# Performance work log

Measured on AMD Instinct MI355X. Metric: run time of the kernel, lower is better.

The kernel has to match this reference:

```python
import jax, jax.numpy as jnp
import numpy as np


def _conv_relu(x, w, b):
    # Conv2d ksize=5, stride=1, padding=2 (same), dilation=1, then ReLU
    y = jax.lax.conv_general_dilated(x, w, window_strides=(1, 1), padding=[(2, 2), (2, 2)],
                                     dimension_numbers=("NCHW", "OIHW", "NCHW"))
    return jax.nn.relu(y + b[None, :, None, None])


def setup_inputs():
    B, S, C, M, BERT = 4, 128, 49, 288, 768
    ks = jax.random.split(jax.random.key(0), 12)
    return {
        "bert_output": jax.random.normal(ks[0], (B, S, BERT), jnp.float32),
        "memory_embs": jax.random.normal(ks[1], (B, S, C, M), jnp.float32),
        "mem_length": jax.random.randint(ks[2], (B, S, 1), 0, C + 1).astype(jnp.int32),
        "cn_concept_weights": jax.random.normal(ks[3], (B, S, C), jnp.float32),
        "ignore_no_memory_token": 1,
        "concept_size": C,
        "W_lin1": jax.random.normal(ks[4], (M, BERT), jnp.float32) * 0.02,
        "b_lin1": jnp.zeros((M,), jnp.float32),
        "sentinel": jax.random.normal(ks[5], (M,), jnp.float32) * 0.02,
        "weight1": jax.random.normal(ks[6], (M, C + 1), jnp.float32) * 0.05,
        "weight2": jax.random.normal(ks[7], (M, C + 1), jnp.float32) * 0.05,
        "conv1_w": jax.random.normal(ks[8], (S, S, 5, 5), jnp.float32) * 0.02,
        "conv1_b": jnp.zeros((S,), jnp.float32),
        "conv2_w": jax.random.normal(ks[9], (S, S, 5, 5), jnp.float32) * 0.02,
        "conv2_b": jnp.zeros((S,), jnp.float32),
        "ln_g": jnp.ones((144,), jnp.float32),
        "ln_b": jnp.zeros((144,), jnp.float32),
        "W_out": jax.random.normal(ks[10], (300, 144), jnp.float32) * 0.05,
        "b_out": jnp.zeros((300,), jnp.float32),
    }


def reference(bert_output, memory_embs, mem_length, cn_concept_weights,
              ignore_no_memory_token, concept_size,
              W_lin1, b_lin1, sentinel, weight1, weight2,
              conv1_w, conv1_b, conv2_w, conv2_b, ln_g, ln_b, W_out, b_out):
    B, S, _ = bert_output.shape
    C = concept_size
    M = sentinel.shape[0]
    eb = bert_output @ W_lin1.T + b_lin1                                   # [B,S,M]
    # add_sentinel: prepend sentinel row, extended_memory [B,S,C+1,M]
    ext_mem = jnp.concatenate([jnp.broadcast_to(sentinel, (B, S, 1, M)), memory_embs], axis=2)
    # expanded_bert[b,s,t,:] = eb[b,t,:]; avoid materializing it via einsum
    attn_w = jnp.einsum("btm,bsjm->bstj", eb, ext_mem)                     # [B,S,S,C+1]
    score = attn_w.mean(axis=2)                                            # [B,S,C+1]
    ordinal = jnp.arange(C + 1, dtype=jnp.float32)
    score = score + (mem_length.astype(jnp.float32) < ordinal).astype(jnp.float32) * (-1e6)
    cw = jnp.concatenate([jnp.zeros((B, S, 1), jnp.float32), cn_concept_weights], axis=2)
    score = 0.7 * jax.nn.softmax(score, axis=2) + 0.3 * jax.nn.softmax(cw, axis=2)
    # top-k threshold mask (keep >= 5th largest), then softmax over masked scores
    thr = jax.lax.top_k(score, 5)[0][..., 4:5]
    score = score * (score >= thr).astype(score.dtype)
    att = jax.nn.softmax(score, axis=2)                                    # [B,S,C+1]
    # torch: matmul of att repeated along last dim with ext_mem
    # == att[...,i] * sum_j ext_mem[...,j,:]
    summ = att[..., None] * ext_mem.sum(axis=2)[:, :, None, :]             # [B,S,C+1,M]
    # einsum 'b s a m, n c -> b s n m' is an outer product of the a-sum with the c-sum
    t1 = summ.sum(axis=2)                                                  # [B,S,M]
    t2 = jnp.einsum("bst,btm->bsm", attn_w.sum(axis=3), eb)                # sum_a (AW^T @ EB)
    cwt = (weight1.sum(axis=1)[None, None, :, None] * t1[:, :, None, :]
           + weight2.sum(axis=1)[None, None, :, None] * t2[:, :, None, :])  # [B,S,M,M]
    cwt = jax.nn.softmax(jnp.tanh(cwt), axis=2)
    summ = jnp.einsum("bsam,bsmn->bsan", summ, cwt)                        # [B,S,C+1,M]
    # self_coding: conv(S->S) -> maxpool2 -> conv -> LayerNorm(144) -> mean over dim2 -> Linear(144,300)
    x = _conv_relu(summ, conv1_w, conv1_b)
    x = jax.lax.reduce_window(x, -jnp.inf, jax.lax.max, (1, 1, 2, 2), (1, 1, 2, 2), "VALID")
    x = _conv_relu(x, conv2_w, conv2_b)                                    # [B,S,(C+1)//2,144]
    mu = x.mean(axis=-1, keepdims=True)
    var = ((x - mu) ** 2).mean(axis=-1, keepdims=True)
    x = (x - mu) / jnp.sqrt(var + 1e-5) * ln_g + ln_b
    x = x.mean(axis=2)                                                     # [B,S,144]
    out = x @ W_out.T + b_out                                              # [B,S,300]
    if ignore_no_memory_token:
        out = out * (mem_length > 0).astype(out.dtype)                     # [B,S,1] broadcast
    return out
```

## Files before the change

kernel.cpp:

```cpp
#include <hip/hip_runtime.h>

#define B_    4
#define S_    128
#define BERT_ 768
#define C_    49
#define C1_   50
#define M_    288
#define HP_   25
#define WP_   144
#define NOUT_ 300

typedef short bf16x8 __attribute__((ext_vector_type(8)));
typedef short short4v __attribute__((ext_vector_type(4)));
typedef float f32x4 __attribute__((ext_vector_type(4)));

static __device__ __forceinline__ short f2bf(float f) {
  unsigned u = __float_as_uint(f);
  unsigned r = (u + 0x7fffu + ((u >> 16) & 1u)) >> 16;
  return (short)r;
}
static __device__ __forceinline__ float bf2f(short v) {
  return __uint_as_float(((unsigned)(unsigned short)v) << 16);
}
static __device__ __forceinline__ unsigned cvt_pk_bf16(float lo, float hi) {
  unsigned r;
  asm("v_cvt_pk_bf16_f32 %0, %1, %2" : "=v"(r) : "v"(lo), "v"(hi));
  return r;
}

static __device__ __forceinline__ void cast_body(const float* src, short* dst,
                                                 long loOff, int R, int Ks, int Kd, int idx)
{
  if (idx >= R * Kd) return;
  int k = idx % Kd, r = idx / Kd;
  short h = 0, l = 0;
  if (k < Ks) {
    float v = src[(long)r * Ks + k];
    h = f2bf(v);
    l = f2bf(v - bf2f(h));
  }
  dst[idx] = h;
  dst[idx + loOff] = l;
}
static __device__ __forceinline__ void wperm_body(const float* w, short* wq, int r)
{
  if (r >= 128 * 128) return;
  int o = r >> 7, ch = r & 127;
  int chq = ch >> 3, e = ch & 7;
  const float* src = &w[(long)r * 25];
#pragma unroll
  for (int tap = 0; tap < 25; ++tap)
    wq[(((long)(tap * 16 + chq)) * 128 + o) * 8 + e] = f2bf(src[tap]);
}
__global__ __launch_bounds__(256) void prep_kernel(
    const float* __restrict__ bert, short* __restrict__ bertb,
    const float* __restrict__ W1, short* __restrict__ w1b,
    const float* __restrict__ Wo, short* __restrict__ wob,
    const float* __restrict__ c1w, short* __restrict__ w1p,
    const float* __restrict__ c2w, short* __restrict__ w2p,
    const float* __restrict__ w1m, const float* __restrict__ w2m,
    float* __restrict__ w1s, float* __restrict__ w2s)
{
  const int g = blockIdx.x, tid = threadIdx.x;
  if (g < 1536)       cast_body(bert, bertb, 393216L, 512, 768, 768, g * 256 + tid);
  else if (g < 2400)  cast_body(W1, w1b, 221184L, 288, 768, 768, (g - 1536) * 256 + tid);
  else if (g < 2700)  cast_body(Wo, wob, 76800L, 300, 144, 256, (g - 2400) * 256 + tid);
  else if (g < 2764)  wperm_body(c1w, w1p, (g - 2700) * 256 + tid);
  else if (g < 2828)  wperm_body(c2w, w2p, (g - 2764) * 256 + tid);
  else {
    int m = (g - 2828) * 256 + tid;
    if (m < M_) {
      float a = 0.f, b = 0.f;
      for (int c = 0; c < C1_; ++c) { a += w1m[m * C1_ + c]; b += w2m[m * C1_ + c]; }
      w1s[m] = a; w2s[m] = b;
    }
  }
}

template<int OMODE>
__global__ __launch_bounds__(256) void gemm_split(
    const short* __restrict__ A, const short* __restrict__ Bm,
    const float* __restrict__ bias,
    float* __restrict__ Outf, short* __restrict__ Outb,
    int Mr, int Nc, int KH,
    long aB, int aP, long aLo,
    long bB, int bP, long bLo,
    long oB, int oP,
    long obB, int obP, long obLo,
    const int* __restrict__ ml, const int* __restrict__ ign)
{
  const int z = blockIdx.z;
  const int i0 = blockIdx.y * 64, j0 = blockIdx.x * 64;
  __shared__ __attribute__((aligned(16))) short As[2][64 * 64];
  __shared__ __attribute__((aligned(16))) short Bs[2][64 * 64];
  const int tid = threadIdx.x;
  const int wave = tid >> 6, lane = tid & 63;
  const int lr = lane & 15, kq = lane >> 4;
  f32x4 acc[4] = {};
  const short* Ab = A + z * aB;
  const short* Bb = Bm + z * bB;
  const bf16x8 vz = {0, 0, 0, 0, 0, 0, 0, 0};
  for (int kh = 0; kh < KH; ++kh) {
    if (kh) __syncthreads();
    for (int u = tid; u < 512; u += 256) {
      int row = u >> 3, c = u & 7;
      int gi = i0 + row;
      const short* src = &Ab[(long)gi * aP + kh * 64 + c * 8];
      bf16x8 vh = (gi < Mr) ? *(const bf16x8*)src : vz;
      bf16x8 vl = (gi < Mr) ? *(const bf16x8*)(src + aLo) : vz;
      int dst = row * 64 + ((c ^ (row & 7)) * 8);
      *(bf16x8*)&As[0][dst] = vh;
      *(bf16x8*)&As[1][dst] = vl;
    }
    for (int u = tid; u < 512; u += 256) {
      int row = u >> 3, c = u & 7;
      int gj = j0 + row;
      const short* src = &Bb[(long)gj * bP + kh * 64 + c * 8];
      bf16x8 vh = (gj < Nc) ? *(const bf16x8*)src : vz;
      bf16x8 vl = (gj < Nc) ? *(const bf16x8*)(src + bLo) : vz;
      int dst = row * 64 + ((c ^ (row & 7)) * 8);
      *(bf16x8*)&Bs[0][dst] = vh;
      *(bf16x8*)&Bs[1][dst] = vl;
    }
    __syncthreads();
#pragma unroll
    for (int ks = 0; ks < 2; ++ks) {
      const int ch = ks * 4 + kq;
      const int ar = wave * 16 + lr;
      const int ao = ar * 64 + ((ch ^ (ar & 7)) * 8);
      bf16x8 ah = *(const bf16x8*)&As[0][ao];
      bf16x8 al = *(const bf16x8*)&As[1][ao];
#pragma unroll
      for (int ni = 0; ni < 4; ++ni) {
        const int br = ni * 16 + lr;
        const int bo2 = br * 64 + ((ch ^ (br & 7)) * 8);
        bf16x8 bh = *(const bf16x8*)&Bs[0][bo2];
        bf16x8 bl = *(const bf16x8*)&Bs[1][bo2];
        acc[ni] = __builtin_amdgcn_mfma_f32_16x16x32_bf16(ah, bh, acc[ni], 0, 0, 0);
        acc[ni] = __builtin_amdgcn_mfma_f32_16x16x32_bf16(ah, bl, acc[ni], 0, 0, 0);
        acc[ni] = __builtin_amdgcn_mfma_f32_16x16x32_bf16(al, bh, acc[ni], 0, 0, 0);
      }
    }
  }
#pragma unroll
  for (int ni = 0; ni < 4; ++ni) {
    int jg = j0 + ni * 16 + lr;
    if (jg >= Nc) continue;
#pragma unroll
    for (int r = 0; r < 4; ++r) {
      int ig = i0 + wave * 16 + kq * 4 + r;
      if (ig >= Mr) continue;
      float v = acc[ni][r];
      if (bias) v += bias[jg];
      if constexpr (OMODE == 0 || OMODE == 1)
        Outf[z * oB + (long)ig * oP + jg] = v;
      if constexpr (OMODE == 1) {
        long o = ((long)((ig >> 7) * 288 + jg)) * 128 + (ig & 127);
        short h = f2bf(v);
        Outb[o] = h;
        Outb[o + obLo] = f2bf(v - bf2f(h));
      }
      if constexpr (OMODE == 2) {
        long o = z * obB + (long)ig * obP + jg;
        short h = f2bf(v);
        Outb[o] = h;
        Outb[o + obLo] = f2bf(v - bf2f(h));
      }
      if constexpr (OMODE == 3) {
        if (ign[0] != 0 && ml[ig] <= 0) v = 0.f;
        Outf[z * oB + (long)ig * oP + jg] = v;
      }
    }
  }
}

__global__ __launch_bounds__(256) void ebbar_kernel(
    const float* __restrict__ eb, float* __restrict__ ebb)
{
  const int chunk = blockIdx.x, b = blockIdx.y;
  const int tid = threadIdx.x;
  const int ml_ = tid & 63, sg = tid >> 6;
  const int m = chunk * 64 + ml_;
  __shared__ float sP[4][64];
  float s = 0.f;
  if (m < M_) {
    const float* p = eb + ((long)(b * S_ + sg * 32)) * M_ + m;
    for (int t = 0; t < 32; ++t) s += p[(long)t * M_];
  }
  sP[sg][ml_] = s;
  __syncthreads();
  if (sg == 0 && m < M_)
    ebb[b * M_ + m] = (sP[0][ml_] + sP[1][ml_] + sP[2][ml_] + sP[3][ml_]) * (1.f / (float)S_);
}

__global__ __launch_bounds__(256) void score_kernel(
    const float* __restrict__ mem, const float* __restrict__ sentinel,
    const float* __restrict__ ebbar, const float* __restrict__ cw,
    const int* __restrict__ ml, float* __restrict__ E, short* __restrict__ Eb,
    float* __restrict__ attTp)
{
  const int s = blockIdx.x, b = blockIdx.y;
  const int tid = threadIdx.x, wave = tid >> 6, lane = tid & 63;
  __shared__ float sEb[M_];
  __shared__ float sE[4][M_];
  __shared__ float sScore[C1_];
  for (int m = tid; m < M_; m += 256) sEb[m] = ebbar[b * M_ + m];
  __syncthreads();

  const float* base = mem + ((long)(b * S_ + s)) * C_ * M_;
  float Ereg[5] = {0.f, 0.f, 0.f, 0.f, 0.f};
  for (int jj = wave; jj < C_; jj += 4) {
    const float* row = base + (long)jj * M_;
    float d = 0.f;
#pragma unroll
    for (int q = 0; q < 5; ++q) {
      int m = lane + q * 64;
      if (m < M_) { float v = row[m]; Ereg[q] += v; d = fmaf(v, sEb[m], d); }
    }
#pragma unroll
    for (int off = 32; off; off >>= 1) d += __shfl_down(d, off, 64);
    if (lane == 0) sScore[jj + 1] = d;
  }
#pragma unroll
  for (int q = 0; q < 5; ++q) { int m = lane + q * 64; if (m < M_) sE[wave][m] = Ereg[q]; }
  __syncthreads();

  if (wave == 0) {
    float d0 = 0.f;
    for (int m = lane; m < M_; m += 64) d0 = fmaf(sentinel[m], sEb[m], d0);
#pragma unroll
    for (int off = 32; off; off >>= 1) d0 += __shfl_down(d0, off, 64);
    if (lane == 0) sScore[0] = d0;
  }
  for (int m = tid; m < M_; m += 256) {
    float ev = sentinel[m] + sE[0][m] + sE[1][m] + sE[2][m] + sE[3][m];
    E[((long)(b * S_ + s)) * M_ + m] = ev;
    short h = f2bf(ev);
    Eb[((long)(b * S_ + s)) * 384 + m] = h;
    Eb[196608 + ((long)(b * S_ + s)) * 384 + m] = f2bf(ev - bf2f(h));
  }
  __syncthreads();

  if (wave == 0) {
    const int mlv = ml[b * S_ + s];
    float sc = (lane < C1_) ? sScore[lane] : 0.f;
    if (lane < C1_ && mlv < lane) sc -= 1e6f;
    float mx = (lane < C1_) ? sc : -3.0e38f;
#pragma unroll
    for (int off = 32; off; off >>= 1) mx = fmaxf(mx, __shfl_xor(mx, off, 64));
    float e1 = (lane < C1_) ? __expf(sc - mx) : 0.f;
    float s1 = e1;
#pragma unroll
    for (int off = 32; off; off >>= 1) s1 += __shfl_xor(s1, off, 64);
    float p1 = e1 / s1;
    float cv = 0.f;
    if (lane >= 1 && lane < C1_) cv = cw[((long)(b * S_ + s)) * C_ + lane - 1];
    float mx2 = (lane < C1_) ? cv : -3.0e38f;
#pragma unroll
    for (int off = 32; off; off >>= 1) mx2 = fmaxf(mx2, __shfl_xor(mx2, off, 64));
    float e2 = (lane < C1_) ? __expf(cv - mx2) : 0.f;
    float s2 = e2;
#pragma unroll
    for (int off = 32; off; off >>= 1) s2 += __shfl_xor(s2, off, 64);
    float p2 = e2 / s2;
    float scm = 0.7f * p1 + 0.3f * p2;
    bool active = (lane < C1_);
    float thr = 0.f;
    for (int r = 0; r < 5; ++r) {
      float v = active ? scm : -3.0e38f;
      int idx = lane;
#pragma unroll
      for (int off = 32; off; off >>= 1) {
        float ov = __shfl_xor(v, off, 64);
        int oi = __shfl_xor(idx, off, 64);
        if (ov > v || (ov == v && oi < idx)) { v = ov; idx = oi; }
      }
      thr = v;
      if (lane == idx) active = false;
    }
    float kept = (lane < C1_ && scm >= thr) ? scm : 0.f;
    float mx3 = (lane < C1_) ? kept : -3.0e38f;
#pragma unroll
    for (int off = 32; off; off >>= 1) mx3 = fmaxf(mx3, __shfl_xor(mx3, off, 64));
    float e3 = (lane < C1_) ? __expf(kept - mx3) : 0.f;
    float s3 = e3;
#pragma unroll
    for (int off = 32; off; off >>= 1) s3 += __shfl_xor(s3, off, 64);
    if (lane < C1_) attTp[((long)(b * 54) + lane + 2) * 128 + s] = e3 / s3;
  }
}

__global__ __launch_bounds__(576) void g_kernel(
    const float* __restrict__ E, const float* __restrict__ t2,
    const float* __restrict__ w1s, const float* __restrict__ w2s,
    short* __restrict__ Gt)
{
  const int s = blockIdx.x, b = blockIdx.y;
  __shared__ float sE[M_], s1[M_], s2[M_];
  const int tid = threadIdx.x;
  const long base = (long)(b * S_ + s) * M_;
  for (int m = tid; m < M_; m += 576) { sE[m] = E[base + m]; s1[m] = w1s[m]; s2[m] = w2s[m]; }
  __syncthreads();
  const int n = tid >> 1, half = tid & 1;
  const float a = sE[n];
  const float c = t2[base + n];
  float num = 0.f, den = 0.f;
  const int m0 = half * 144;
#pragma unroll 4
  for (int mm = 0; mm < 144; ++mm) {
    int m = m0 + mm;
    float z = fmaf(s1[m], a, s2[m] * c);
    float u = __expf(2.f * z);
    float th = 1.f - 2.f / (u + 1.f);
    float e = __expf(th);
    num = fmaf(sE[m], e, num);
    den += e;
  }
  num += __shfl_xor(num, 1, 64);
  den += __shfl_xor(den, 1, 64);
  if (half == 0)
    Gt[((long)(b * 292) + 2 + n) * 128 + s] = f2bf(num / den);
}

__global__ __launch_bounds__(256) void conv1_aw(
    const short* __restrict__ w1q, const float* __restrict__ attp,
    short* __restrict__ AWq)
{
  const int b = blockIdx.z, h = blockIdx.y, half = blockIdx.x;
  __shared__ float sAtt[5][128];
  const int tid = threadIdx.x;
  for (int u = tid; u < 640; u += 256)
    sAtt[u >> 7][u & 127] = attp[((long)(b * 54) + h + (u >> 7)) * 128 + (u & 127)];
  __syncthreads();
  const long obase = ((long)(b * 50 + h) * 80) * 1024;
  for (int u = tid; u < 5120; u += 256) {
    int c = half * 40 + (u >> 7);
    int o = u & 127;
    int dw = c / 16, chq = c & 15;
    float acc[8] = {};
#pragma unroll
    for (int dh = 0; dh < 5; ++dh) {
      bf16x8 wv = *(const bf16x8*)&w1q[(((long)((dh * 5 + dw) * 16 + chq)) * 128 + o) * 8];
      const float* ar = &sAtt[dh][chq * 8];
#pragma unroll
      for (int e = 0; e < 8; ++e) acc[e] = fmaf(bf2f(wv[e]), ar[e], acc[e]);
    }
    union { unsigned u4[4]; bf16x8 v; } pk;
    pk.u4[0] = cvt_pk_bf16(acc[0], acc[1]);
    pk.u4[1] = cvt_pk_bf16(acc[2], acc[3]);
    pk.u4[2] = cvt_pk_bf16(acc[4], acc[5]);
    pk.u4[3] = cvt_pk_bf16(acc[6], acc[7]);
    *(bf16x8*)&AWq[obase + (long)c * 1024 + o * 8] = pk.v;
  }
}

__global__ __launch_bounds__(256) void conv1_mfma(
    const short* __restrict__ AWq, const short* __restrict__ Gt,
    const float* __restrict__ bias, short* __restrict__ y1t)
{
  const int b = blockIdx.z, hrow = blockIdx.y;
  const int w0 = blockIdx.x * 144;
  __shared__ __attribute__((aligned(16))) short Bs[2][148 * 64];
  const int tid = threadIdx.x;
  const int wave = tid >> 6, lane = tid & 63;
  const int lr = lane & 15, kq = lane >> 4;
  f32x4 acc[2][9] = {};

  const short* src = Gt + ((long)(b * 292) + w0) * 128;
  for (int u = tid; u < 2368; u += 256) {
    int row = u >> 4, c = u & 15;
    bf16x8 v = *(const bf16x8*)&src[row * 128 + c * 8];
    *(bf16x8*)&Bs[c >> 3][row * 64 + (((c & 7) ^ (row & 7)) * 8)] = v;
  }
  __syncthreads();

  const long awb = (long)(b * 50 + hrow) * 80;
  for (int dw = 0; dw < 5; ++dw) {
#pragma unroll
    for (int ks = 0; ks < 4; ++ks) {
      const int ch = ks * 4 + kq;
      const long abase = (awb + dw * 16 + ch) * 128 + wave * 32 + lr;
      bf16x8 af0 = *(const bf16x8*)&AWq[abase * 8];
      bf16x8 af1 = *(const bf16x8*)&AWq[(abase + 16) * 8];
      const int arr = ch >> 3, cc = ch & 7;
#pragma unroll
      for (int ni = 0; ni < 9; ++ni) {
        const int row = lr + ni * 16 + dw;
        bf16x8 bfr = *(const bf16x8*)&Bs[arr][row * 64 + ((cc ^ (row & 7)) * 8)];
        acc[0][ni] = __builtin_amdgcn_mfma_f32_16x16x32_bf16(af0, bfr, acc[0][ni], 0, 0, 0);
        acc[1][ni] = __builtin_amdgcn_mfma_f32_16x16x32_bf16(af1, bfr, acc[1][ni], 0, 0, 0);
      }
    }
  }
#pragma unroll
  for (int mi = 0; mi < 2; ++mi) {
    const int og = wave * 32 + mi * 16 + kq * 4;
#pragma unroll
    for (int ni = 0; ni < 9; ++ni) {
      int wg = w0 + ni * 16 + lr;
      short4v pk;
#pragma unroll
      for (int r = 0; r < 4; ++r)
        pk[r] = f2bf(fmaxf(acc[mi][ni][r] + bias[og + r], 0.f));
      *(short4v*)&y1t[(((long)(b * 50) + hrow) * 288 + wg) * 128 + og] = pk;
    }
  }
}

__global__ __launch_bounds__(256) void conv2_dh(
    const short* __restrict__ wq,
    const short* __restrict__ act,
    short* __restrict__ y2p)
{
  constexpr int NREP = 3;
  const int bz = blockIdx.z;
  const int b = bz / 5, dh = bz % 5;
  const int hp = blockIdx.y;
  const int w0 = blockIdx.x * 48;
  __shared__ __attribute__((aligned(16))) short Bs[2][52 * 64];
  const int tid = threadIdx.x;
  const int wave = tid >> 6, lane = tid & 63;
  const int lr = lane & 15, kq = lane >> 4;
  f32x4 acc[2][NREP] = {};

  const short* src = act + (((long)(b * 29) + hp + dh) * 148 + w0) * 128;
  for (int u = tid; u < 832; u += 256) {
    int row = u >> 4, c = u & 15;
    bf16x8 v = *(const bf16x8*)&src[row * 128 + c * 8];
    *(bf16x8*)&Bs[c >> 3][row * 64 + (((c & 7) ^ (row & 7)) * 8)] = v;
  }
  __syncthreads();

#pragma unroll
  for (int dw = 0; dw < 5; ++dw) {
    const int tap = dh * 5 + dw;
#pragma unroll
    for (int ks = 0; ks < 4; ++ks) {
      const int ch = ks * 4 + kq;
      const long abase = ((long)(tap * 16 + ch)) * 128 + wave * 32 + lr;
      bf16x8 af0 = *(const bf16x8*)&wq[abase * 8];
      bf16x8 af1 = *(const bf16x8*)&wq[(abase + 16) * 8];
      const int arr = ch >> 3, cc = ch & 7;
#pragma unroll
      for (int ni = 0; ni < NREP; ++ni) {
        const int row = lr + ni * 16 + dw;
        bf16x8 bfr = *(const bf16x8*)&Bs[arr][row * 64 + ((cc ^ (row & 7)) * 8)];
        acc[0][ni] = __builtin_amdgcn_mfma_f32_16x16x32_bf16(af0, bfr, acc[0][ni], 0, 0, 0);
        acc[1][ni] = __builtin_amdgcn_mfma_f32_16x16x32_bf16(af1, bfr, acc[1][ni], 0, 0, 0);
      }
    }
  }
#pragma unroll
  for (int mi = 0; mi < 2; ++mi) {
    const int og = wave * 32 + mi * 16 + kq * 4;
#pragma unroll
    for (int ni = 0; ni < NREP; ++ni) {
      int wg = w0 + ni * 16 + lr;
#pragma unroll
      for (int r = 0; r < 4; ++r)
        y2p[((long)(dh * 512 + b * 128 + og + r)) * 3600 + hp * 144 + wg] =
            f2bf(acc[mi][ni][r]);
    }
  }
}

__global__ __launch_bounds__(256) void tail_fuse(
    const short* __restrict__ y2p, const float* __restrict__ bias,
    const float* __restrict__ lng, const float* __restrict__ lnb,
    short* __restrict__ zb)
{
  const int o = blockIdx.x, b = blockIdx.y;
  const int tid = threadIdx.x, wave = tid >> 6, lane = tid & 63;
  __shared__ float sZ[4][3][64];
  float zacc[3] = {0.f, 0.f, 0.f};
  const float bo = bias[o];
  const long base = ((long)(b * 128 + o)) * 3600;
  for (int hp = wave; hp < HP_; hp += 4) {
    float v[3]; float s = 0.f, ss = 0.f;
#pragma unroll
    for (int q = 0; q < 3; ++q) {
      int wp = lane + q * 64;
      float x = 0.f;
      if (wp < WP_) {
        x = bo;
#pragma unroll
        for (int dh = 0; dh < 5; ++dh)
          x += bf2f(y2p[(long)dh * 512 * 3600 + base + hp * 144 + wp]);
        x = fmaxf(x, 0.f);
      }
      v[q] = x; s += x; ss = fmaf(x, x, ss);
    }
#pragma unroll
    for (int off = 32; off; off >>= 1) { s += __shfl_xor(s, off, 64); ss += __shfl_xor(ss, off, 64); }
    float mu = s * (1.f / (float)WP_);
    float var = ss * (1.f / (float)WP_) - mu * mu;
    float inv = rsqrtf(var + 1e-5f);
#pragma unroll
    for (int q = 0; q < 3; ++q) {
      int wp = lane + q * 64;
      if (wp < WP_) zacc[q] += (v[q] - mu) * inv * lng[wp] + lnb[wp];
    }
  }
#pragma unroll
  for (int q = 0; q < 3; ++q) sZ[wave][q][lane] = zacc[q];
  __syncthreads();
  if (wave == 0) {
#pragma unroll
    for (int q = 0; q < 3; ++q) {
      int wp = lane + q * 64;
      if (wp < WP_) {
        float z = (sZ[0][q][lane] + sZ[1][q][lane] + sZ[2][q][lane] + sZ[3][q][lane])
                  * (1.f / (float)HP_);
        long t = (long)(b * 128 + o);
        short h = f2bf(z);
        zb[t * 256 + wp] = h;
        zb[131072 + t * 256 + wp] = f2bf(z - bf2f(h));
      }
    }
  }
}

__global__ void pool_t(const short* __restrict__ y1t, short* __restrict__ x2t)
{
  int idx = blockIdx.x * 256 + threadIdx.x;
  if (idx >= B_ * HP_ * WP_ * 16) return;
  int c8 = idx & 15; int t = idx >> 4;
  int wp = t % WP_; t /= WP_;
  int hp = t % HP_; int b = t / HP_;
  const short* base = y1t + (((long)(b * 50 + 2 * hp) * 288) + 2 * wp) * 128 + c8 * 8;
  bf16x8 v00 = *(const bf16x8*)&base[0];
  bf16x8 v01 = *(const bf16x8*)&base[128];
  bf16x8 v10 = *(const bf16x8*)&base[288 * 128];
  bf16x8 v11 = *(const bf16x8*)&base[288 * 128 + 128];
  bf16x8 r;
#pragma unroll
  for (int e = 0; e < 8; ++e)
    r[e] = f2bf(fmaxf(fmaxf(bf2f(v00[e]), bf2f(v01[e])), fmaxf(bf2f(v10[e]), bf2f(v11[e]))));
  *(bf16x8*)&x2t[(((long)(b * 29) + hp + 2) * 148 + wp + 2) * 128 + c8 * 8] = r;
}

extern "C" void kernel_launch(void* const* d_in, const int* in_sizes, int n_in,
                              void* d_out, int out_size, void* d_ws, size_t ws_size,
                              hipStream_t stream)
{
  const float* bert = (const float*)d_in[0];
  const float* mem  = (const float*)d_in[1];
  const int*   ml   = (const int*)d_in[2];
  const float* cw   = (const float*)d_in[3];
  const int*   ign  = (const int*)d_in[4];
  const float* W1   = (const float*)d_in[6];
  const float* b1l  = (const float*)d_in[7];
  const float* sent = (const float*)d_in[8];
  const float* w1m  = (const float*)d_in[9];
  const float* w2m  = (const float*)d_in[10];
  const float* c1w  = (const float*)d_in[11];
  const float* c1b  = (const float*)d_in[12];
  const float* c2w  = (const float*)d_in[13];
  const float* c2b  = (const float*)d_in[14];
  const float* lng  = (const float*)d_in[15];
  const float* lnb  = (const float*)d_in[16];
  const float* Wo   = (const float*)d_in[17];
  const float* bo   = (const float*)d_in[18];
  float* out = (float*)d_out;

  short* Gt    = (short*)d_ws;
  short* x2t   = Gt + 149504;
  short* zb    = x2t + 2197504;
  float* attTp = (float*)(zb + 262144);
  float* w1s   = attTp + 27648;
  float* w2s   = w1s + 288;
  float* ebb   = w2s + 288;
  short* wob   = (short*)(ebb + 1152);
  short* w1p   = wob + 153600;
  short* w2p   = w1p + 409600;
  short* y1t   = w2p + 409600;
  short* poolX = y1t + 7372800;
  short* bertb = poolX;
  short* w1b   = bertb + 786432;
  short* ebt   = w1b + 442368;
  short* Eb    = ebt + 294912;
  short* pb    = Eb + 393216;
  float* ebf   = (float*)(pb + 884736);
  float* E     = ebf + 147456;
  float* t2    = E + 147456;
  short* AWq   = poolX;
  short* y2p   = poolX;

  dim3 blk(256);

  hipMemsetAsync(Gt, 0, (size_t)5328896, stream);
  hipMemsetAsync(Eb, 0, (size_t)(393216 + 884736) * 2, stream);

  prep_kernel<<<dim3(2830), blk, 0, stream>>>(
      bert, bertb, W1, w1b, Wo, wob, c1w, w1p, c2w, w2p, w1m, w2m, w1s, w2s);

  gemm_split<1><<<dim3(5, 8, 1), blk, 0, stream>>>(
      bertb, w1b, b1l, ebf, ebt, 512, 288, 12,
      0L, 768, 393216L, 0L, 768, 221184L, 0L, 288, 0L, 0, 147456L,
      (const int*)nullptr, (const int*)nullptr);

  ebbar_kernel<<<dim3(5, 4), blk, 0, stream>>>(ebf, ebb);

  score_kernel<<<dim3(S_, B_), blk, 0, stream>>>(mem, sent, ebb, cw, ml, E, Eb, attTp);

  gemm_split<2><<<dim3(5, 5, 4), blk, 0, stream>>>(
      ebt, ebt, (const float*)nullptr, (float*)nullptr, pb, 288, 288, 2,
      (long)288 * 128, 128, 147456L, (long)288 * 128, 128, 147456L,
      0L, 0, (long)288 * 384, 384, 442368L,
      (const int*)nullptr, (const int*)nullptr);

  gemm_split<0><<<dim3(5, 2, 4), blk, 0, stream>>>(
      Eb, pb, (const float*)nullptr, t2, (short*)nullptr, 128, 288, 6,
      (long)128 * 384, 384, 196608L, (long)288 * 384, 384, 442368L,
      (long)128 * 288, 288, 0L, 0, 0L,
      (const int*)nullptr, (const int*)nullptr);

  g_kernel<<<dim3(S_, B_), dim3(576), 0, stream>>>(E, t2, w1s, w2s, Gt);

  conv1_aw<<<dim3(2, 50, 4), blk, 0, stream>>>(w1p, attTp, AWq);
  conv1_mfma<<<dim3(2, 50, 4), blk, 0, stream>>>(AWq, Gt, c1b, y1t);

  pool_t<<<dim3((B_ * HP_ * WP_ * 16 + 255) / 256), blk, 0, stream>>>(y1t, x2t);

  conv2_dh<<<dim3(3, 25, 20), blk, 0, stream>>>(w2p, x2t, y2p);

  tail_fuse<<<dim3(128, 4), blk, 0, stream>>>(y2p, c2b, lng, lnb, zb);

  gemm_split<3><<<dim3(5, 8, 1), blk, 0, stream>>>(
      zb, wob, bo, out, (short*)nullptr, 512, 300, 4,
      0L, 256, 131072L, 0L, 256, 76800L, 0L, 300, 0L, 0, 0L,
      ml, ign);
}
```

Measured before the change: 204.3 us.

## Fuse conv1 weight-activation product into MFMA conv kernel via shared memory

Merges the conv1_aw kernel, which wrote per-row combined weights AWq to global memory, into the conv1 MFMA kernel. Each block now recomputes the 16x128x8 weight slice for each dw into LDS, then runs the MFMAs from LDS. The column tile also shrinks from 144 to 96 (grid 3 instead of 2) to fit the extra LDS. This removes a global write and read round trip and one launch, but each block redoes the AW computation (3x redundant across the column tiles) and adds barriers per dw step.

Result: slower. 223.6 us (+9.4%).

```diff
diff --git a/kernel.cpp b/kernel.cpp
--- a/kernel.cpp
+++ b/kernel.cpp
@@ -322,69 +322,63 @@
     Gt[((long)(b * 292) + 2 + n) * 128 + s] = f2bf(num / den);
 }
 
-__global__ __launch_bounds__(256) void conv1_aw(
+__global__ __launch_bounds__(256) void conv1_fused(
     const short* __restrict__ w1q, const float* __restrict__ attp,
-    short* __restrict__ AWq)
-{
-  const int b = blockIdx.z, h = blockIdx.y, half = blockIdx.x;
+    const short* __restrict__ Gt, const float* __restrict__ bias,
+    short* __restrict__ y1t)
+{
+  constexpr int NREP = 6;
+  constexpr int ROWS = 100;
+  const int b = blockIdx.z, hrow = blockIdx.y;
+  const int w0 = blockIdx.x * 96;
   __shared__ float sAtt[5][128];
-  const int tid = threadIdx.x;
-  for (int u = tid; u < 640; u += 256)
-    sAtt[u >> 7][u & 127] = attp[((long)(b * 54) + h + (u >> 7)) * 128 + (u & 127)];
-  __syncthreads();
-  const long obase = ((long)(b * 50 + h) * 80) * 1024;
-  for (int u = tid; u < 5120; u += 256) {
-    int c = half * 40 + (u >> 7);
-    int o = u & 127;
-    int dw = c / 16, chq = c & 15;
-    float acc[8] = {};
-#pragma unroll
-    for (int dh = 0; dh < 5; ++dh) {
-      bf16x8 wv = *(const bf16x8*)&w1q[(((long)((dh * 5 + dw) * 16 + chq)) * 128 + o) * 8];
-      const float* ar = &sAtt[dh][chq * 8];
-#pragma unroll
-      for (int e = 0; e < 8; ++e) acc[e] = fmaf(bf2f(wv[e]), ar[e], acc[e]);
-    }
-    union { unsigned u4[4]; bf16x8 v; } pk;
-    pk.u4[0] = cvt_pk_bf16(acc[0], acc[1]);
-    pk.u4[1] = cvt_pk_bf16(acc[2], acc[3]);
-    pk.u4[2] = cvt_pk_bf16(acc[4], acc[5]);
-    pk.u4[3] = cvt_pk_bf16(acc[6], acc[7]);
-    *(bf16x8*)&AWq[obase + (long)c * 1024 + o * 8] = pk.v;
-  }
-}
-
-__global__ __launch_bounds__(256) void conv1_mfma(
-    const short* __restrict__ AWq, const short* __restrict__ Gt,
-    const float* __restrict__ bias, short* __restrict__ y1t)
-{
-  const int b = blockIdx.z, hrow = blockIdx.y;
-  const int w0 = blockIdx.x * 144;
-  __shared__ __attribute__((aligned(16))) short Bs[2][148 * 64];
+  __shared__ __attribute__((aligned(16))) short Bs[2][ROWS * 64];
+  __shared__ __attribute__((aligned(16))) short aw[16 * 128 * 8];
   const int tid = threadIdx.x;
   const int wave = tid >> 6, lane = tid & 63;
   const int lr = lane & 15, kq = lane >> 4;
-  f32x4 acc[2][9] = {};
-
-  const short* src = Gt + ((long)(b * 292) + w0) * 128;
-  for (int u = tid; u < 2368; u += 256) {
-    int row = u >> 4, c = u & 15;
-    bf16x8 v = *(const bf16x8*)&src[row * 128 + c * 8];
-    *(bf16x8*)&Bs[c >> 3][row * 64 + (((c & 7) ^ (row & 7)) * 8)] = v;
-  }
-  __syncthreads();
-
-  const long awb = (long)(b * 50 + hrow) * 80;
+  f32x4 acc[2][NREP] = {};
+
+  for (int u = tid; u < 640; u += 256)
+    sAtt[u >> 7][u & 127] = attp[((long)(b * 54) + hrow + (u >> 7)) * 128 + (u & 127)];
+  {
+    const short* src = Gt + ((long)(b * 292) + w0) * 128;
+    for (int u = tid; u < ROWS * 16; u += 256) {
+      int row = u >> 4, c = u & 15;
+      bf16x8 v = *(const bf16x8*)&src[row * 128 + c * 8];
+      *(bf16x8*)&Bs[c >> 3][row * 64 + (((c & 7) ^ (row & 7)) * 8)] = v;
+    }
+  }
+  __syncthreads();
+
   for (int dw = 0; dw < 5; ++dw) {
+    if (dw) __syncthreads();
+    for (int u = tid; u < 2048; u += 256) {
+      int chq = u >> 7, o = u & 127;
+      float a8[8] = {};
+#pragma unroll
+      for (int dh = 0; dh < 5; ++dh) {
+        bf16x8 wv = *(const bf16x8*)&w1q[(((long)((dh * 5 + dw) * 16 + chq)) * 128 + o) * 8];
+        const float* ar = &sAtt[dh][chq * 8];
+#pragma unroll
+        for (int e = 0; e < 8; ++e) a8[e] = fmaf(bf2f(wv[e]), ar[e], a8[e]);
+      }
+      union { unsigned u4[4]; bf16x8 v; } pk;
+      pk.u4[0] = cvt_pk_bf16(a8[0], a8[1]);
+      pk.u4[1] = cvt_pk_bf16(a8[2], a8[3]);
+      pk.u4[2] = cvt_pk_bf16(a8[4], a8[5]);
+      pk.u4[3] = cvt_pk_bf16(a8[6], a8[7]);
+      *(bf16x8*)&aw[(chq * 128 + o) * 8] = pk.v;
+    }
+    __syncthreads();
 #pragma unroll
     for (int ks = 0; ks < 4; ++ks) {
       const int ch = ks * 4 + kq;
-      const long abase = (awb + dw * 16 + ch) * 128 + wave * 32 + lr;
-      bf16x8 af0 = *(const bf16x8*)&AWq[abase * 8];
-      bf16x8 af1 = *(const bf16x8*)&AWq[(abase + 16) * 8];
+      bf16x8 af0 = *(const bf16x8*)&aw[(ch * 128 + wave * 32 + lr) * 8];
+      bf16x8 af1 = *(const bf16x8*)&aw[(ch * 128 + wave * 32 + 16 + lr) * 8];
       const int arr = ch >> 3, cc = ch & 7;
 #pragma unroll
-      for (int ni = 0; ni < 9; ++ni) {
+      for (int ni = 0; ni < NREP; ++ni) {
         const int row = lr + ni * 16 + dw;
         bf16x8 bfr = *(const bf16x8*)&Bs[arr][row * 64 + ((cc ^ (row & 7)) * 8)];
         acc[0][ni] = __builtin_amdgcn_mfma_f32_16x16x32_bf16(af0, bfr, acc[0][ni], 0, 0, 0);
@@ -396,7 +390,7 @@
   for (int mi = 0; mi < 2; ++mi) {
     const int og = wave * 32 + mi * 16 + kq * 4;
 #pragma unroll
-    for (int ni = 0; ni < 9; ++ni) {
+    for (int ni = 0; ni < NREP; ++ni) {
       int wg = w0 + ni * 16 + lr;
       short4v pk;
 #pragma unroll
@@ -583,7 +577,6 @@
   float* ebf   = (float*)(pb + 884736);
   float* E     = ebf + 147456;
   float* t2    = E + 147456;
-  short* AWq   = poolX;
   short* y2p   = poolX;
 
   dim3 blk(256);
@@ -617,8 +610,7 @@
 
   g_kernel<<<dim3(S_, B_), dim3(576), 0, stream>>>(E, t2, w1s, w2s, Gt);
 
-  conv1_aw<<<dim3(2, 50, 4), blk, 0, stream>>>(w1p, attTp, AWq);
-  conv1_mfma<<<dim3(2, 50, 4), blk, 0, stream>>>(AWq, Gt, c1b, y1t);
+  conv1_fused<<<dim3(3, 50, 4), blk, 0, stream>>>(w1p, attTp, Gt, c1b, y1t);
 
   pool_t<<<dim3((B_ * HP_ * WP_ * 16 + 255) / 256), blk, 0, stream>>>(y1t, x2t);
 
```
